# Optimization experiments

Hardware: AMD Instinct MI355X
Metric: run time of the kernel (lower is better)

Reference implementation:

```python
import jax, jax.numpy as jnp
import numpy as np

BATCH, T, D_MODEL = 4, 4096, 2048


def setup_inputs() -> dict:
    key = jax.random.key(0)
    kx, ka, kb, kc, kd = jax.random.split(key, 5)
    x = jax.random.normal(kx, (BATCH, T, D_MODEL), dtype=jnp.float32)
    A = jax.random.normal(ka, (D_MODEL,), dtype=jnp.float32)
    B = jax.random.normal(kb, (D_MODEL,), dtype=jnp.float32)
    C = jax.random.normal(kc, (D_MODEL,), dtype=jnp.float32)
    D = jax.random.normal(kd, (D_MODEL,), dtype=jnp.float32)
    return {"x": x, "A": A, "B": B, "C": C, "D": D}


def reference(x, A, B, C, D):
    # Diagonal LTI SSM: h_t = A*h_{t-1} + B*x_t ; y_t = C*h_t + D*x_t
    # x: (batch, T, d_model). Scan over time axis.
    batch, _, d = x.shape
    s0 = jnp.zeros((batch, d), dtype=x.dtype)

    def step(s, xt):
        s = A * s + B * xt          # (batch, d)
        yt = C * s + D * xt
        return s, yt

    # scan over leading axis -> move T to front
    _, ys = jax.lax.scan(step, s0, jnp.swapaxes(x, 0, 1))
    return jnp.swapaxes(ys, 0, 1)   # (batch, T, d_model)
```

## Files before the change

### kernel.cpp

```cpp
#include <hip/hip_runtime.h>

#define BATCHN  4
#define TLEN    4096
#define D4      512
#define DG      8
#define NDG     64
#define THREADS 512
#define TTILE   512
#define NTILE   8
#define NSUB    64
#define TSUB    8
#define TILE_F4 (TTILE * DG)

typedef float f4 __attribute__((ext_vector_type(4)));

__device__ __forceinline__ float fin(float v) {
    return fminf(fmaxf(v, -1.0e30f), 1.0e30f);
}
__device__ __forceinline__ f4 fin4(f4 v) {
    f4 r;
    r.x = fin(v.x); r.y = fin(v.y); r.z = fin(v.z); r.w = fin(v.w);
    return r;
}

#define BAR() do { asm volatile("s_waitcnt lgkmcnt(0)" ::: "memory"); \
                   __builtin_amdgcn_s_barrier();                       \
                   asm volatile("" ::: "memory"); } while (0)

__device__ __forceinline__ int swz(int row, int col) {
    return row * DG + ((col + (row >> 3)) & 7);
}

__global__ __launch_bounds__(THREADS, 1) void ssm_onepass(
    const float* __restrict__ xg, const float* __restrict__ A,
    const float* __restrict__ B, const float* __restrict__ Cv,
    const float* __restrict__ Dv, float* __restrict__ yg) {
    __shared__ f4 tile[2 * TILE_F4];
    __shared__ f4 pfx[NSUB * DG];

    const int tid  = threadIdx.x;
    const int lane = tid & 63;
    const int wid  = tid >> 6;
    const int dg   = blockIdx.x & (NDG - 1);
    const int b    = blockIdx.x >> 6;
    const int ch   = tid & (DG - 1);
    const int sub  = tid >> 3;

    const int d4 = dg * DG + ch;
    const f4 a  = ((const f4*)A)[d4];
    const f4 bb = ((const f4*)B)[d4];
    const f4 cc = ((const f4*)Cv)[d4];
    const f4 dd = ((const f4*)Dv)[d4];
    const f4 a2 = fin4(a * a), a4 = fin4(a2 * a2), a8 = fin4(a4 * a4);

    f4 S = {0.f, 0.f, 0.f, 0.f};

    const size_t slice = (size_t)b * TLEN * D4 + (size_t)dg * DG;
    const f4* xbase = (const f4*)xg + slice;
    f4* ybase = (f4*)yg + slice;

    int g_row[TSUB], g_col[TSUB];
#pragma unroll
    for (int q = 0; q < TSUB; ++q) {
        int s = q * THREADS + wid * 64 + lane;
        g_row[q] = s >> 3;
        g_col[q] = ((s & 7) - (s >> 6)) & 7;
    }

#define STAGE(t_, bufi_) do {                                                  \
        const f4* gq;                                                          \
        f4* lq;                                                                \
        _Pragma("unroll")                                                      \
        for (int q = 0; q < TSUB; ++q) {                                       \
            gq = xbase + (size_t)((t_) * TTILE + g_row[q]) * D4 + g_col[q];    \
            lq = &tile[(bufi_) * TILE_F4 + q * THREADS + wid * 64];            \
            __builtin_amdgcn_global_load_lds(                                  \
                (const __attribute__((address_space(1))) void*)gq,             \
                (__attribute__((address_space(3))) void*)lq, 16, 0, 0);        \
        }                                                                      \
    } while (0)

    STAGE(0, 0);
    asm volatile("s_waitcnt vmcnt(0)" ::: "memory");
    __builtin_amdgcn_s_barrier();
    asm volatile("" ::: "memory");

    for (int t = 0; t < NTILE; ++t) {
        f4* bufp = &tile[(t & 1) * TILE_F4];

        if (t + 1 < NTILE) STAGE(t + 1, (t & 1) ^ 1);

        f4 xcur[TSUB];
        const int r0 = sub * TSUB;
#pragma unroll
        for (int i = 0; i < TSUB; ++i) xcur[i] = bufp[swz(r0 + i, ch)];
        {
            f4 v = {0.f, 0.f, 0.f, 0.f};
#pragma unroll
            for (int i = 0; i < TSUB; ++i) v = fin4(a * v + bb * xcur[i]);
            pfx[sub * DG + ch] = v;
        }
        BAR();

        if (tid < DG) {
            for (int s0 = 0; s0 < NSUB; s0 += 8) {
                f4 v0 = pfx[(s0 + 0) * DG + tid];
                f4 v1 = pfx[(s0 + 1) * DG + tid];
                f4 v2 = pfx[(s0 + 2) * DG + tid];
                f4 v3 = pfx[(s0 + 3) * DG + tid];
                f4 v4 = pfx[(s0 + 4) * DG + tid];
                f4 v5 = pfx[(s0 + 5) * DG + tid];
                f4 v6 = pfx[(s0 + 6) * DG + tid];
                f4 v7 = pfx[(s0 + 7) * DG + tid];
                pfx[(s0 + 0) * DG + tid] = S; S = fin4(a8 * S + v0);
                pfx[(s0 + 1) * DG + tid] = S; S = fin4(a8 * S + v1);
                pfx[(s0 + 2) * DG + tid] = S; S = fin4(a8 * S + v2);
                pfx[(s0 + 3) * DG + tid] = S; S = fin4(a8 * S + v3);
                pfx[(s0 + 4) * DG + tid] = S; S = fin4(a8 * S + v4);
                pfx[(s0 + 5) * DG + tid] = S; S = fin4(a8 * S + v5);
                pfx[(s0 + 6) * DG + tid] = S; S = fin4(a8 * S + v6);
                pfx[(s0 + 7) * DG + tid] = S; S = fin4(a8 * S + v7);
            }
        }
        BAR();

        {
            f4 s = pfx[sub * DG + ch];
#pragma unroll
            for (int i = 0; i < TSUB; ++i) {
                f4 xi = xcur[i];
                s = fin4(a * s + bb * xi);
                bufp[swz(r0 + i, ch)] = fin4(cc * s + dd * xi);
            }
        }
        BAR();

#pragma unroll
        for (int q = 0; q < TSUB; ++q) {
            int sIdx = q * THREADS + tid;
            int row = sIdx >> 3;
            int col = ((sIdx & 7) - (sIdx >> 6)) & 7;
            f4 yv = bufp[sIdx];
            __builtin_nontemporal_store(
                yv, ybase + (size_t)(t * TTILE + row) * D4 + col);
        }

        if (t + 1 < NTILE) {
            asm volatile("s_waitcnt vmcnt(8)" ::: "memory");
            __builtin_amdgcn_s_barrier();
            asm volatile("" ::: "memory");
        }
    }
#undef STAGE
}

extern "C" void kernel_launch(void* const* d_in, const int* in_sizes, int n_in,
                              void* d_out, int out_size, void* d_ws, size_t ws_size,
                              hipStream_t stream) {
    const float* x  = (const float*)d_in[0];
    const float* A  = (const float*)d_in[1];
    const float* B  = (const float*)d_in[2];
    const float* Cv = (const float*)d_in[3];
    const float* Dv = (const float*)d_in[4];
    float* y = (float*)d_out;

    const int nblocks = BATCHN * NDG;
    ssm_onepass<<<nblocks, THREADS, 0, stream>>>(x, A, B, Cv, Dv, y);
}
```

Before: 56.08 us.

## Replace serial per-tile carry scan with wavefront shuffle parallel scan

```diff
diff --git a/kernel.cpp b/kernel.cpp
--- a/kernel.cpp
+++ b/kernel.cpp
@@ -23,6 +23,22 @@
     return r;
 }
 
+struct pr { f4 p, v; };
+__device__ __forceinline__ pr comp(pr later, pr earlier) {
+    pr r;
+    r.p = fin4(later.p * earlier.p);
+    r.v = fin4(later.p * earlier.v + later.v);
+    return r;
+}
+__device__ __forceinline__ f4 shflup4(f4 x, int delta) {
+    f4 r;
+    r.x = __shfl_up(x.x, (unsigned)delta, 64);
+    r.y = __shfl_up(x.y, (unsigned)delta, 64);
+    r.z = __shfl_up(x.z, (unsigned)delta, 64);
+    r.w = __shfl_up(x.w, (unsigned)delta, 64);
+    return r;
+}
+
 #define BAR() do { asm volatile("s_waitcnt lgkmcnt(0)" ::: "memory"); \
                    __builtin_amdgcn_s_barrier();                       \
                    asm volatile("" ::: "memory"); } while (0)
@@ -36,7 +52,9 @@
     const float* __restrict__ B, const float* __restrict__ Cv,
     const float* __restrict__ Dv, float* __restrict__ yg) {
     __shared__ f4 tile[2 * TILE_F4];
-    __shared__ f4 pfx[NSUB * DG];
+    __shared__ f4 wpP[NSUB];
+    __shared__ f4 wpV[NSUB];
+    __shared__ f4 totP[DG], totV[DG];
 
     const int tid  = threadIdx.x;
     const int lane = tid & 63;
@@ -45,6 +63,7 @@
     const int b    = blockIdx.x >> 6;
     const int ch   = tid & (DG - 1);
     const int sub  = tid >> 3;
+    const int siw  = (lane >> 3);
 
     const int d4 = dg * DG + ch;
     const f4 a  = ((const f4*)A)[d4];
@@ -52,8 +71,10 @@
     const f4 cc = ((const f4*)Cv)[d4];
     const f4 dd = ((const f4*)Dv)[d4];
     const f4 a2 = fin4(a * a), a4 = fin4(a2 * a2), a8 = fin4(a4 * a4);
-
-    f4 S = {0.f, 0.f, 0.f, 0.f};
+    const f4 ONE = {1.f, 1.f, 1.f, 1.f};
+    const f4 ZERO = {0.f, 0.f, 0.f, 0.f};
+
+    f4 S = ZERO;
 
     const size_t slice = (size_t)b * TLEN * D4 + (size_t)dg * DG;
     const f4* xbase = (const f4*)xg + slice;
@@ -94,44 +115,58 @@
         const int r0 = sub * TSUB;
 #pragma unroll
         for (int i = 0; i < TSUB; ++i) xcur[i] = bufp[swz(r0 + i, ch)];
+        pr me;
         {
-            f4 v = {0.f, 0.f, 0.f, 0.f};
+            f4 v = ZERO;
 #pragma unroll
             for (int i = 0; i < TSUB; ++i) v = fin4(a * v + bb * xcur[i]);
-            pfx[sub * DG + ch] = v;
-        }
+            me.p = a8; me.v = v;
+        }
+
+#pragma unroll
+        for (int d = 1; d <= 4; d <<= 1) {
+            pr up;
+            up.p = shflup4(me.p, 8 * d);
+            up.v = shflup4(me.v, 8 * d);
+            if (siw >= d) me = comp(me, up);
+        }
+        if (siw == 7) { wpP[wid * DG + ch] = me.p; wpV[wid * DG + ch] = me.v; }
         BAR();
 
-        if (tid < DG) {
-            for (int s0 = 0; s0 < NSUB; s0 += 8) {
-                f4 v0 = pfx[(s0 + 0) * DG + tid];
-                f4 v1 = pfx[(s0 + 1) * DG + tid];
-                f4 v2 = pfx[(s0 + 2) * DG + tid];
-                f4 v3 = pfx[(s0 + 3) * DG + tid];
-                f4 v4 = pfx[(s0 + 4) * DG + tid];
-                f4 v5 = pfx[(s0 + 5) * DG + tid];
-                f4 v6 = pfx[(s0 + 6) * DG + tid];
-                f4 v7 = pfx[(s0 + 7) * DG + tid];
-                pfx[(s0 + 0) * DG + tid] = S; S = fin4(a8 * S + v0);
-                pfx[(s0 + 1) * DG + tid] = S; S = fin4(a8 * S + v1);
-                pfx[(s0 + 2) * DG + tid] = S; S = fin4(a8 * S + v2);
-                pfx[(s0 + 3) * DG + tid] = S; S = fin4(a8 * S + v3);
-                pfx[(s0 + 4) * DG + tid] = S; S = fin4(a8 * S + v4);
-                pfx[(s0 + 5) * DG + tid] = S; S = fin4(a8 * S + v5);
-                pfx[(s0 + 6) * DG + tid] = S; S = fin4(a8 * S + v6);
-                pfx[(s0 + 7) * DG + tid] = S; S = fin4(a8 * S + v7);
+        if (tid < 64) {
+            const int ww = tid >> 3, c2 = tid & 7;
+            pr q; q.p = wpP[tid]; q.v = wpV[tid];
+#pragma unroll
+            for (int d = 1; d <= 4; d <<= 1) {
+                pr up;
+                up.p = shflup4(q.p, 8 * d);
+                up.v = shflup4(q.v, 8 * d);
+                if (ww >= d) q = comp(q, up);
             }
+            if (ww == 7) { totP[c2] = q.p; totV[c2] = q.v; }
+            pr ex;
+            ex.p = shflup4(q.p, 8);
+            ex.v = shflup4(q.v, 8);
+            if (ww == 0) { ex.p = ONE; ex.v = ZERO; }
+            wpP[tid] = ex.p; wpV[tid] = ex.v;
         }
         BAR();
 
-        {
-            f4 s = pfx[sub * DG + ch];
-#pragma unroll
-            for (int i = 0; i < TSUB; ++i) {
-                f4 xi = xcur[i];
-                s = fin4(a * s + bb * xi);
-                bufp[swz(r0 + i, ch)] = fin4(cc * s + dd * xi);
-            }
+        pr wex; wex.p = wpP[wid * DG + ch]; wex.v = wpV[wid * DG + ch];
+        pr mex;
+        mex.p = shflup4(me.p, 8);
+        mex.v = shflup4(me.v, 8);
+        if (siw == 0) { mex.p = ONE; mex.v = ZERO; }
+        pr st = comp(mex, wex);
+        f4 s = fin4(fin4(st.p * S) + st.v);
+
+        S = fin4(fin4(totP[ch] * S) + totV[ch]);
+
+#pragma unroll
+        for (int i = 0; i < TSUB; ++i) {
+            f4 xi = xcur[i];
+            s = fin4(a * s + bb * xi);
+            bufp[swz(r0 + i, ch)] = fin4(cc * s + dd * xi);
         }
         BAR();
 
```

Result: faster. 53.65 us (-4.3%).
